# Kernel tuning notes

Hardware: AMD Instinct MI355X
Metric: run time of the kernel (lower is better)

## Reference

```python
import jax, jax.numpy as jnp
import numpy as np

B, IN_C, NHEAD, ATT_C, OUT_C, H, W = 512, 256, 8, 32, 32, 19, 19
EPS = 1e-5


def setup_inputs() -> dict:
    key = jax.random.key(0)
    ks = jax.random.split(key, 4)
    f32 = jnp.float32
    return {
        "x": jax.random.normal(ks[0], (B, IN_C, H, W), f32),
        "Wq": jax.random.normal(ks[1], (NHEAD * ATT_C, IN_C), f32) * 0.05,
        "bq": jnp.zeros((NHEAD * ATT_C,), f32),
        "Wk": jax.random.normal(ks[2], (NHEAD * ATT_C, IN_C), f32) * 0.05,
        "bk": jnp.zeros((NHEAD * ATT_C,), f32),
        "Wv": jax.random.normal(ks[3], (NHEAD * OUT_C, IN_C), f32) * 0.05,
        "bv": jnp.zeros((NHEAD * OUT_C,), f32),
        "gQ": jnp.ones((NHEAD * ATT_C,), f32),
        "betaQ": jnp.zeros((NHEAD * ATT_C,), f32),
        "gK": jnp.ones((NHEAD * ATT_C,), f32),
        "betaK": jnp.zeros((NHEAD * ATT_C,), f32),
        "gV": jnp.ones((NHEAD * OUT_C,), f32),
        "betaV": jnp.zeros((NHEAD * OUT_C,), f32),
    }


def _conv1x1(x, Wt, bt):
    # x: [B,Ci,H,W], Wt: [Co,Ci] -> [B,Co,H,W]
    return jnp.einsum("oi,bihw->bohw", Wt, x) + bt[None, :, None, None]


def _bn(x, g, b):
    # training-mode BatchNorm2d: batch stats over (N,H,W)
    mu = x.mean(axis=(0, 2, 3), keepdims=True)
    var = x.var(axis=(0, 2, 3), keepdims=True)
    return (x - mu) * jax.lax.rsqrt(var + EPS) * g[None, :, None, None] + b[None, :, None, None]


def _neighbors(t):
    # t: [B,C,H,W] -> [B,4,C,H,W] zero-padded 4-neighbor shifts (up,down,left,right)
    p = jnp.pad(t, ((0, 0), (0, 0), (1, 1), (1, 1)))
    return jnp.stack(
        (p[:, :, 0:-2, 1:-1], p[:, :, 2:, 1:-1], p[:, :, 1:-1, 0:-2], p[:, :, 1:-1, 2:]),
        axis=1,
    )


def reference(x, Wq, bq, Wk, bk, Wv, bv, gQ, betaQ, gK, betaK, gV, betaV):
    Q = _bn(_conv1x1(x, Wq, bq), gQ, betaQ)
    K = _bn(_conv1x1(x, Wk, bk), gK, betaK)
    V = _bn(_conv1x1(x, Wv, bv), gV, betaV)

    Kn = _neighbors(K).reshape(B, 4, NHEAD, ATT_C, H, W)
    Q4 = Q.reshape(B, 1, NHEAD, ATT_C, H, W)
    # attention logits: mean over att_c, then * sqrt(att_c)  (usenormmean == 0)
    a = (Q4 * Kn).mean(axis=3) * jnp.float32(ATT_C ** 0.5)  # [B,4,nhead,H,W]
    a = jax.nn.softmax(a, axis=1)[:, :, :, None]  # [B,4,nhead,1,H,W]

    Vn = _neighbors(V).reshape(B, 4, NHEAD, OUT_C, H, W)
    out = (a * Vn).sum(axis=1)  # [B,nhead,out_c,H,W]
    out = out.reshape(B, NHEAD * OUT_C, H, W)
    out = jax.nn.relu(out)  # useRelu == 1
    return out + x  # residual
```

## Files before the change

kernel.cpp:

```cpp
#include <hip/hip_runtime.h>

typedef unsigned short u16;
typedef unsigned int   u32;

#define NB     512
#define NHEADS 8
#define HW     361
#define NPIX   184832
#define NTOT   768
#define EPSBN  1e-5f
#define RS     0.17677669529663687f
#define PSTR   104

typedef __bf16 bf16x8 __attribute__((ext_vector_type(8)));
typedef float  f32x4  __attribute__((ext_vector_type(4)));

__device__ __forceinline__ u16 f2bf(float f) {
  u32 u = __float_as_uint(f);
  u += 0x7fffu + ((u >> 16) & 1u);
  return (u16)(u >> 16);
}
__device__ __forceinline__ float bf2f(u16 v) {
  return __uint_as_float(((u32)v) << 16);
}
__device__ __forceinline__ bf16x8 ldb8(const void* p) {
  return __builtin_bit_cast(bf16x8, *(const uint4*)p);
}
__device__ __forceinline__ float dot2(u32 a, u32 b) {
  return bf2f((u16)a) * bf2f((u16)b) + bf2f((u16)(a >> 16)) * bf2f((u16)(b >> 16));
}
__device__ __forceinline__ float dot8(uint4 a, uint4 b) {
  return dot2(a.x, b.x) + dot2(a.y, b.y) + dot2(a.z, b.z) + dot2(a.w, b.w);
}

__global__ __launch_bounds__(256) void k_prep(
    const float* __restrict__ Wq, const float* __restrict__ bq,
    const float* __restrict__ Wk, const float* __restrict__ bk,
    const float* __restrict__ Wv, const float* __restrict__ bv,
    u16* __restrict__ Wall, float* __restrict__ ball,
    float* __restrict__ sx) {
  const int n = blockIdx.x, t = threadIdx.x;
  const float* src; const float* bs; int r;
  if (n < 256)      { src = Wq; bs = bq; r = n; }
  else if (n < 512) { src = Wk; bs = bk; r = n - 256; }
  else              { src = Wv; bs = bv; r = n - 512; }
  Wall[n * 256 + t] = f2bf(src[r * 256 + t]);
  if (t == 0) ball[n] = bs[r];
  if (n == 0) sx[t] = 0.f;
}

__global__ __launch_bounds__(512) void k_M(
    const float* __restrict__ x, u16* __restrict__ xT,
    float* __restrict__ Mpart, float* __restrict__ sx) {
  __shared__ u16 Als[256 * 64];
  const int tid = threadIdx.x, g = blockIdx.x;
  const int lane = tid & 63, w = tid >> 6;
  const int l15 = lane & 15, kq = lane >> 4;
  const int sc  = tid >> 4;
  const int sq  = tid & 15;
  const int wpx = tid & 63;
  const int wcs = tid >> 6;
  char* Ab = (char*)Als;

  float sxp[8];
  f32x4 acc[2][16];
  #pragma unroll
  for (int i = 0; i < 8; ++i) sxp[i] = 0.f;
  #pragma unroll
  for (int f2 = 0; f2 < 16; ++f2) {
    acc[0][f2] = (f32x4){0.f, 0.f, 0.f, 0.f};
    acc[1][f2] = (f32x4){0.f, 0.f, 0.f, 0.f};
  }

  #pragma unroll 1
  for (int ch = 0; ch < 12; ++ch) {
    const int img = (ch >= 6) ? 1 : 0;
    const int px0 = (ch - img * 6) * 64;
    const int bb  = g * 2 + img;
    const int pb  = px0 + sq * 4;
    #pragma unroll
    for (int i = 0; i < 8; ++i) {
      const int c = sc + 32 * i;
      const float* xp = x + ((size_t)bb * 256 + c) * HW + pb;
      float v0, v1, v2, v3;
      if (pb + 3 < HW) {
        const float4 f4 = *(const float4*)xp;
        v0 = f4.x; v1 = f4.y; v2 = f4.z; v3 = f4.w;
      } else {
        v0 = (pb + 0 < HW) ? xp[0] : 0.f;
        v1 = (pb + 1 < HW) ? xp[1] : 0.f;
        v2 = (pb + 2 < HW) ? xp[2] : 0.f;
        v3 = (pb + 3 < HW) ? xp[3] : 0.f;
      }
      sxp[i] += v0 + v1 + v2 + v3;
      const u32 lo = (u32)f2bf(v0) | ((u32)f2bf(v1) << 16);
      const u32 hi = (u32)f2bf(v2) | ((u32)f2bf(v3) << 16);
      const int slot = (sq >> 1) ^ (c & 7);
      *(uint2*)(Ab + c * 128 + slot * 16 + (sq & 1) * 8) = make_uint2(lo, hi);
    }
    __syncthreads();
    #pragma unroll
    for (int kk = 0; kk < 2; ++kk) {
      const int gl = kk * 4 + kq;
      const int so = ((gl ^ (l15 & 7)) << 4);
      const int r0 = w * 32 + l15;
      const bf16x8 a0 = ldb8(Ab + r0 * 128 + so);
      const bf16x8 a1 = ldb8(Ab + (r0 + 16) * 128 + so);
      #pragma unroll
      for (int f2 = 0; f2 < 16; ++f2) {
        const bf16x8 b = ldb8(Ab + (f2 * 16 + l15) * 128 + so);
        acc[0][f2] = __builtin_amdgcn_mfma_f32_16x16x32_bf16(a0, b, acc[0][f2], 0, 0, 0);
        acc[1][f2] = __builtin_amdgcn_mfma_f32_16x16x32_bf16(a1, b, acc[1][f2], 0, 0, 0);
      }
    }
    const int pxg = px0 + wpx;
    if (pxg < HW) {
      __align__(16) u16 tmp[32];
      #pragma unroll
      for (int j = 0; j < 32; ++j) {
        const int c = wcs * 32 + j;
        tmp[j] = Als[c * 64 + (((wpx >> 3) ^ (c & 7)) << 3) + (wpx & 7)];
      }
      uint4* dst = (uint4*)(xT + ((size_t)bb * HW + pxg) * 256 + wcs * 32);
      dst[0] = ((const uint4*)tmp)[0];
      dst[1] = ((const uint4*)tmp)[1];
      dst[2] = ((const uint4*)tmp)[2];
      dst[3] = ((const uint4*)tmp)[3];
    }
    __syncthreads();
  }
  float* mp = Mpart + (size_t)g * 65536;
  #pragma unroll
  for (int f1 = 0; f1 < 2; ++f1)
    #pragma unroll
    for (int f2 = 0; f2 < 16; ++f2)
      #pragma unroll
      for (int j = 0; j < 4; ++j) {
        const int c1 = w * 32 + f1 * 16 + kq * 4 + j;
        const int c2 = f2 * 16 + l15;
        mp[c1 * 256 + c2] = acc[f1][f2][j];
      }
  #pragma unroll
  for (int i = 0; i < 8; ++i) {
    float v = sxp[i];
    v += __shfl_down(v, 8); v += __shfl_down(v, 4);
    v += __shfl_down(v, 2); v += __shfl_down(v, 1);
    if (sq == 0) atomicAdd(&sx[sc + 32 * i], v);
  }
}

__global__ __launch_bounds__(256) void k_red(const float* __restrict__ Mpart,
                                             float* __restrict__ Mg) {
  const int i = blockIdx.x * 256 + threadIdx.x;
  float s = 0.f;
  #pragma unroll 8
  for (int sl = 0; sl < 256; ++sl) s += Mpart[(size_t)sl * 65536 + i];
  Mg[i] = s;
}

__global__ __launch_bounds__(256) void k_stats2(
    const float* __restrict__ Mg, const float* __restrict__ sx,
    const float* __restrict__ Wq, const float* __restrict__ bq,
    const float* __restrict__ Wk, const float* __restrict__ bk,
    const float* __restrict__ Wv, const float* __restrict__ bv,
    const float* __restrict__ gQ, const float* __restrict__ betaQ,
    const float* __restrict__ gK, const float* __restrict__ betaK,
    const float* __restrict__ gV, const float* __restrict__ betaV,
    float* __restrict__ s_all, float* __restrict__ t_all) {
  __shared__ float ws[256];
  __shared__ float r1[4], r2[4];
  const int n = blockIdx.x, i = threadIdx.x;
  const int which = n >> 8, r = n & 255;
  const float* src = (which == 0) ? Wq : (which == 1) ? Wk : Wv;
  const float wi = src[r * 256 + i];
  ws[i] = wi;
  __syncthreads();
  float colsum = 0.f;
  #pragma unroll 4
  for (int j = 0; j < 256; ++j) colsum += Mg[j * 256 + i] * ws[j];
  float p1 = wi * sx[i];
  float p2 = wi * colsum;
  p1 += __shfl_down(p1, 32); p2 += __shfl_down(p2, 32);
  p1 += __shfl_down(p1, 16); p2 += __shfl_down(p2, 16);
  p1 += __shfl_down(p1, 8);  p2 += __shfl_down(p2, 8);
  p1 += __shfl_down(p1, 4);  p2 += __shfl_down(p2, 4);
  p1 += __shfl_down(p1, 2);  p2 += __shfl_down(p2, 2);
  p1 += __shfl_down(p1, 1);  p2 += __shfl_down(p2, 1);
  const int wv = i >> 6;
  if ((i & 63) == 0) { r1[wv] = p1; r2[wv] = p2; }
  __syncthreads();
  if (i == 0) {
    const float S1 = r1[0] + r1[1] + r1[2] + r1[3];
    const float S2 = r2[0] + r2[1] + r2[2] + r2[3];
    const float* bs = (which == 0) ? bq : (which == 1) ? bk : bv;
    const float* gs = (which == 0) ? gQ : (which == 1) ? gK : gV;
    const float* be = (which == 0) ? betaQ : (which == 1) ? betaK : betaV;
    const float b = bs[r];
    const float P = (float)NPIX;
    const float mean = (S1 + P * b) / P;
    const float Ey2  = (S2 + 2.f * b * S1 + P * b * b) / P;
    const float var  = Ey2 - mean * mean;
    const float s    = gs[r] * rsqrtf(var + EPSBN);
    s_all[n] = s;
    t_all[n] = be[r] - s * mean;
  }
}

__global__ __launch_bounds__(768) void k_fused(
    const u16* __restrict__ xT, const u16* __restrict__ Wall,
    const float* __restrict__ ball,
    const float* __restrict__ s_all, const float* __restrict__ t_all,
    const float* __restrict__ x, float* __restrict__ out) {
  __shared__ u16   Wl[96 * 256];
  __shared__ __align__(16) u16 P[HW * PSTR];
  __shared__ float aL[4 * HW];
  __shared__ float stl[2 * 96];
  const int tid = threadIdx.x;
  const int wg  = blockIdx.x;
  const int xcd = wg & 7, ii = wg >> 3;
  const int h   = ii & 7;
  const int pr  = xcd * 32 + (ii >> 3);
  const int bb0 = pr * 2;
  const char* Pb = (const char*)P;

  const int lane = tid & 63, wv = tid >> 6;
  const int l15 = lane & 15, kq = lane >> 4;

  const bool pact = tid < 2 * HW;
  const int  ppx  = pact ? ((tid < HW) ? tid : tid - HW) : 0;
  const int  poc0 = (tid < HW) ? 0 : 16;

  uint4 bfr[16];
  {
    const u16* xTb = xT + (size_t)bb0 * HW * 256;
    #pragma unroll
    for (int ks = 0; ks < 8; ++ks) {
      bfr[2 * ks]     = *(const uint4*)(xTb + (size_t)(wv * 32      + l15) * 256 + ks * 32 + kq * 8);
      bfr[2 * ks + 1] = *(const uint4*)(xTb + (size_t)(wv * 32 + 16 + l15) * 256 + ks * 32 + kq * 8);
    }
  }
  float xres[16];
  if (pact) {
    const size_t pg = ((size_t)bb0 * 256 + h * 32 + poc0) * HW + ppx;
    #pragma unroll
    for (int o = 0; o < 16; ++o) xres[o] = x[pg + (size_t)o * HW];
  }
  if (tid < 96) {
    const int which = tid >> 5, c32 = tid & 31;
    const int n = which * 256 + h * 32 + c32;
    float s = s_all[n];
    float t = s * ball[n] + t_all[n];
    if (tid < 32) { s *= RS; t *= RS; }
    stl[tid] = s; stl[96 + tid] = t;
  }
  #pragma unroll
  for (int i = 0; i < 4; ++i) {
    const int gi = tid + i * 768;
    const int lr = gi >> 5, gg = gi & 31;
    const int which = lr >> 5, c32 = lr & 31;
    uint4 v = *(const uint4*)(Wall + (size_t)(which * 256 + h * 32 + c32) * 256 + gg * 8);
    const int slot = gg ^ (lr & 7);
    *(uint4*)((char*)Wl + lr * 512 + slot * 16) = v;
  }
  __syncthreads();

  #pragma unroll
  for (int im = 0; im < 2; ++im) {
    const int bb = bb0 + im;
    f32x4 acc[6][2];
    #pragma unroll
    for (int f = 0; f < 6; ++f) {
      acc[f][0] = (f32x4){0.f, 0.f, 0.f, 0.f};
      acc[f][1] = (f32x4){0.f, 0.f, 0.f, 0.f};
    }
    #pragma unroll
    for (int ks = 0; ks < 8; ++ks) {
      bf16x8 b0 = __builtin_bit_cast(bf16x8, bfr[2 * ks]);
      bf16x8 b1 = __builtin_bit_cast(bf16x8, bfr[2 * ks + 1]);
      const int slot = ((ks * 4 + kq) ^ (l15 & 7)) * 16;
      #pragma unroll
      for (int f = 0; f < 6; ++f) {
        const int lr = (f >> 1) * 32 + (f & 1) * 16 + l15;
        bf16x8 a = ldb8((const char*)Wl + lr * 512 + slot);
        acc[f][0] = __builtin_amdgcn_mfma_f32_16x16x32_bf16(a, b0, acc[f][0], 0, 0, 0);
        acc[f][1] = __builtin_amdgcn_mfma_f32_16x16x32_bf16(a, b1, acc[f][1], 0, 0, 0);
      }
    }
    if (im == 0) {
      const u16* xTb2 = xT + (size_t)(bb0 + 1) * HW * 256;
      #pragma unroll
      for (int ks = 0; ks < 8; ++ks) {
        bfr[2 * ks]     = *(const uint4*)(xTb2 + (size_t)(wv * 32      + l15) * 256 + ks * 32 + kq * 8);
        bfr[2 * ks + 1] = *(const uint4*)(xTb2 + (size_t)(wv * 32 + 16 + l15) * 256 + ks * 32 + kq * 8);
      }
    }
    #pragma unroll
    for (int f = 0; f < 6; ++f) {
      const int ch0 = f * 16 + kq * 4;
      const float s0 = stl[ch0], t0 = stl[96 + ch0];
      const float s1 = stl[ch0 + 1], t1 = stl[96 + ch0 + 1];
      const float s2 = stl[ch0 + 2], t2 = stl[96 + ch0 + 2];
      const float s3 = stl[ch0 + 3], t3 = stl[96 + ch0 + 3];
      #pragma unroll
      for (int p2 = 0; p2 < 2; ++p2) {
        const int px = wv * 32 + p2 * 16 + l15;
        if (px < HW) {
          const u32 lo = (u32)f2bf(s0 * acc[f][p2][0] + t0)
                       | ((u32)f2bf(s1 * acc[f][p2][1] + t1) << 16);
          const u32 hi = (u32)f2bf(s2 * acc[f][p2][2] + t2)
                       | ((u32)f2bf(s3 * acc[f][p2][3] + t3) << 16);
          *(uint2*)((char*)P + px * 208 + f * 32 + kq * 8) = make_uint2(lo, hi);
        }
      }
    }
    __syncthreads();

    if (tid < HW) {
      const int px = tid;
      const int yy = px / 19, xx = px - yy * 19;
      const bool i0 = yy > 0, i1 = yy < 18, i2 = xx > 0, i3 = xx < 18;
      const int pn0 = i0 ? px - 19 : px, pn1 = i1 ? px + 19 : px;
      const int pn2 = i2 ? px - 1  : px, pn3 = i3 ? px + 1  : px;
      const uint4* Qp = (const uint4*)(Pb + px * 208);
      const uint4 q0 = Qp[0], q1 = Qp[1], q2 = Qp[2], q3 = Qp[3];
      const uint4* K0 = (const uint4*)(Pb + pn0 * 208 + 64);
      const uint4* K1 = (const uint4*)(Pb + pn1 * 208 + 64);
      const uint4* K2 = (const uint4*)(Pb + pn2 * 208 + 64);
      const uint4* K3 = (const uint4*)(Pb + pn3 * 208 + 64);
      float l0 = dot8(q0, K0[0]) + dot8(q1, K0[1]) + dot8(q2, K0[2]) + dot8(q3, K0[3]);
      float l1 = dot8(q0, K1[0]) + dot8(q1, K1[1]) + dot8(q2, K1[2]) + dot8(q3, K1[3]);
      float l2 = dot8(q0, K2[0]) + dot8(q1, K2[1]) + dot8(q2, K2[2]) + dot8(q3, K2[3]);
      float l3 = dot8(q0, K3[0]) + dot8(q1, K3[1]) + dot8(q2, K3[2]) + dot8(q3, K3[3]);
      l0 = i0 ? l0 : 0.f; l1 = i1 ? l1 : 0.f;
      l2 = i2 ? l2 : 0.f; l3 = i3 ? l3 : 0.f;
      const float mx = fmaxf(fmaxf(l0, l1), fmaxf(l2, l3));
      const float e0 = __expf(l0 - mx), e1 = __expf(l1 - mx);
      const float e2 = __expf(l2 - mx), e3 = __expf(l3 - mx);
      const float inv = 1.f / (e0 + e1 + e2 + e3);
      aL[0 * HW + px] = i0 ? e0 * inv : 0.f;
      aL[1 * HW + px] = i1 ? e1 * inv : 0.f;
      aL[2 * HW + px] = i2 ? e2 * inv : 0.f;
      aL[3 * HW + px] = i3 ? e3 * inv : 0.f;
    }
    __syncthreads();

    if (pact) {
      const int px = ppx;
      const size_t pgb = ((size_t)bb * 256 + h * 32 + poc0) * HW + px;
      const int yy = px / 19, xx = px - yy * 19;
      const int pn0 = (yy > 0)  ? px - 19 : px, pn1 = (yy < 18) ? px + 19 : px;
      const int pn2 = (xx > 0)  ? px - 1  : px, pn3 = (xx < 18) ? px + 1  : px;
      const float a0 = aL[0 * HW + px], a1 = aL[1 * HW + px];
      const float a2 = aL[2 * HW + px], a3 = aL[3 * HW + px];
      const int vb = 128 + poc0 * 2;
      const uint4* V0 = (const uint4*)(Pb + pn0 * 208 + vb);
      const uint4* V1 = (const uint4*)(Pb + pn1 * 208 + vb);
      const uint4* V2 = (const uint4*)(Pb + pn2 * 208 + vb);
      const uint4* V3 = (const uint4*)(Pb + pn3 * 208 + vb);
      #pragma unroll
      for (int half = 0; half < 2; ++half) {
        const uint4 w0 = V0[half], w1 = V1[half], w2 = V2[half], w3 = V3[half];
        const u32 u0[4] = {w0.x, w0.y, w0.z, w0.w};
        const u32 u1[4] = {w1.x, w1.y, w1.z, w1.w};
        const u32 u2[4] = {w2.x, w2.y, w2.z, w2.w};
        const u32 u3[4] = {w3.x, w3.y, w3.z, w3.w};
        #pragma unroll
        for (int p = 0; p < 4; ++p) {
          const int o = half * 8 + p * 2;
          float vlo = a0 * bf2f((u16)u0[p]) + a1 * bf2f((u16)u1[p])
                    + a2 * bf2f((u16)u2[p]) + a3 * bf2f((u16)u3[p]);
          float vhi = a0 * bf2f((u16)(u0[p] >> 16)) + a1 * bf2f((u16)(u1[p] >> 16))
                    + a2 * bf2f((u16)(u2[p] >> 16)) + a3 * bf2f((u16)(u3[p] >> 16));
          vlo = fmaxf(vlo, 0.f);
          vhi = fmaxf(vhi, 0.f);
          out[pgb + (size_t)o * HW]       = vlo + xres[o];
          out[pgb + (size_t)(o + 1) * HW] = vhi + xres[o + 1];
        }
      }
    }
    if (im == 0 && pact) {
      const size_t pg2 = ((size_t)(bb0 + 1) * 256 + h * 32 + poc0) * HW + ppx;
      #pragma unroll
      for (int o = 0; o < 16; ++o) xres[o] = x[pg2 + (size_t)o * HW];
    }
    __syncthreads();
  }
}

constexpr size_t OFF_XT    = 0;
constexpr size_t SZ_XT     = (size_t)NPIX * 512 + 16384;
constexpr size_t OFF_WALL  = OFF_XT + SZ_XT;
constexpr size_t SZ_WALL   = (size_t)NTOT * 512;
constexpr size_t OFF_BALL  = OFF_WALL + SZ_WALL;
constexpr size_t OFF_M     = OFF_BALL + NTOT * 4;
constexpr size_t SZ_M      = 256 * 256 * 4;
constexpr size_t OFF_SX    = OFF_M + SZ_M;
constexpr size_t OFF_SALL  = OFF_SX + 256 * 4;
constexpr size_t OFF_TALL  = OFF_SALL + NTOT * 4;
constexpr size_t OFF_MPART = OFF_TALL + NTOT * 4;
constexpr size_t SZ_MPART  = (size_t)256 * 65536 * 4;
constexpr size_t WS_NEEDED = OFF_MPART + SZ_MPART;

extern "C" void kernel_launch(void* const* d_in, const int* in_sizes, int n_in,
                              void* d_out, int out_size, void* d_ws, size_t ws_size,
                              hipStream_t stream) {
  (void)in_sizes; (void)n_in; (void)out_size;
  if (ws_size < WS_NEEDED) return;

  const float* x     = (const float*)d_in[0];
  const float* Wq    = (const float*)d_in[1];
  const float* bq    = (const float*)d_in[2];
  const float* Wk    = (const float*)d_in[3];
  const float* bk    = (const float*)d_in[4];
  const float* Wv    = (const float*)d_in[5];
  const float* bv    = (const float*)d_in[6];
  const float* gQ    = (const float*)d_in[7];
  const float* betaQ = (const float*)d_in[8];
  const float* gK    = (const float*)d_in[9];
  const float* betaK = (const float*)d_in[10];
  const float* gV    = (const float*)d_in[11];
  const float* betaV = (const float*)d_in[12];
  float* out = (float*)d_out;

  char* wsp = (char*)d_ws;
  u16*   xT    = (u16*)(wsp + OFF_XT);
  u16*   Wall  = (u16*)(wsp + OFF_WALL);
  float* ball  = (float*)(wsp + OFF_BALL);
  float* Mg    = (float*)(wsp + OFF_M);
  float* sx    = (float*)(wsp + OFF_SX);
  float* s_all = (float*)(wsp + OFF_SALL);
  float* t_all = (float*)(wsp + OFF_TALL);
  float* Mpart = (float*)(wsp + OFF_MPART);

  k_prep<<<NTOT, 256, 0, stream>>>(Wq, bq, Wk, bk, Wv, bv, Wall, ball, sx);
  k_M<<<256, 512, 0, stream>>>(x, xT, Mpart, sx);
  k_red<<<256, 256, 0, stream>>>(Mpart, Mg);
  k_stats2<<<NTOT, 256, 0, stream>>>(Mg, sx, Wq, bq, Wk, bk, Wv, bv,
                                     gQ, betaQ, gK, betaK, gV, betaV, s_all, t_all);
  k_fused<<<2048, 768, 0, stream>>>(xT, Wall, ball, s_all, t_all, x, out);
}
```

Baseline: 375.9 us.

## Split Gram-matrix kernel across two blocks per image pair with XCD-aware mapping

```diff
diff --git a/kernel.cpp b/kernel.cpp
--- a/kernel.cpp
+++ b/kernel.cpp
@@ -10,7 +10,6 @@
 #define NTOT   768
 #define EPSBN  1e-5f
 #define RS     0.17677669529663687f
-#define PSTR   104
 
 typedef __bf16 bf16x8 __attribute__((ext_vector_type(8)));
 typedef float  f32x4  __attribute__((ext_vector_type(4)));
@@ -53,7 +52,11 @@
     const float* __restrict__ x, u16* __restrict__ xT,
     float* __restrict__ Mpart, float* __restrict__ sx) {
   __shared__ u16 Als[256 * 64];
-  const int tid = threadIdx.x, g = blockIdx.x;
+  const int tid  = threadIdx.x;
+  const int orig = blockIdx.x;
+  const int xcd  = orig & 7, kk8 = orig >> 3;
+  const int g    = xcd * 32 + (kk8 >> 1);
+  const int half = kk8 & 1;
   const int lane = tid & 63, w = tid >> 6;
   const int l15 = lane & 15, kq = lane >> 4;
   const int sc  = tid >> 4;
@@ -61,16 +64,14 @@
   const int wpx = tid & 63;
   const int wcs = tid >> 6;
   char* Ab = (char*)Als;
+  const int c1base = half * 128 + w * 16;
 
   float sxp[8];
-  f32x4 acc[2][16];
+  f32x4 acc[16];
   #pragma unroll
   for (int i = 0; i < 8; ++i) sxp[i] = 0.f;
   #pragma unroll
-  for (int f2 = 0; f2 < 16; ++f2) {
-    acc[0][f2] = (f32x4){0.f, 0.f, 0.f, 0.f};
-    acc[1][f2] = (f32x4){0.f, 0.f, 0.f, 0.f};
-  }
+  for (int f2 = 0; f2 < 16; ++f2) acc[f2] = (f32x4){0.f, 0.f, 0.f, 0.f};
 
   #pragma unroll 1
   for (int ch = 0; ch < 12; ++ch) {
@@ -79,73 +80,78 @@
     const int bb  = g * 2 + img;
     const int pb  = px0 + sq * 4;
     #pragma unroll
-    for (int i = 0; i < 8; ++i) {
-      const int c = sc + 32 * i;
-      const float* xp = x + ((size_t)bb * 256 + c) * HW + pb;
-      float v0, v1, v2, v3;
-      if (pb + 3 < HW) {
-        const float4 f4 = *(const float4*)xp;
-        v0 = f4.x; v1 = f4.y; v2 = f4.z; v3 = f4.w;
-      } else {
-        v0 = (pb + 0 < HW) ? xp[0] : 0.f;
-        v1 = (pb + 1 < HW) ? xp[1] : 0.f;
-        v2 = (pb + 2 < HW) ? xp[2] : 0.f;
-        v3 = (pb + 3 < HW) ? xp[3] : 0.f;
-      }
-      sxp[i] += v0 + v1 + v2 + v3;
-      const u32 lo = (u32)f2bf(v0) | ((u32)f2bf(v1) << 16);
-      const u32 hi = (u32)f2bf(v2) | ((u32)f2bf(v3) << 16);
-      const int slot = (sq >> 1) ^ (c & 7);
-      *(uint2*)(Ab + c * 128 + slot * 16 + (sq & 1) * 8) = make_uint2(lo, hi);
+    for (int b4 = 0; b4 < 2; ++b4) {
+      float4 fv[4];
+      #pragma unroll
+      for (int i2 = 0; i2 < 4; ++i2) {
+        const int c = sc + 32 * (b4 * 4 + i2);
+        const float* xp = x + ((size_t)bb * 256 + c) * HW + pb;
+        if (pb + 3 < HW) {
+          fv[i2] = *(const float4*)xp;
+        } else {
+          fv[i2].x = (pb + 0 < HW) ? xp[0] : 0.f;
+          fv[i2].y = (pb + 1 < HW) ? xp[1] : 0.f;
+          fv[i2].z = (pb + 2 < HW) ? xp[2] : 0.f;
+          fv[i2].w = (pb + 3 < HW) ? xp[3] : 0.f;
+        }
+      }
+      #pragma unroll
+      for (int i2 = 0; i2 < 4; ++i2) {
+        const int i = b4 * 4 + i2;
+        const int c = sc + 32 * i;
+        sxp[i] += fv[i2].x + fv[i2].y + fv[i2].z + fv[i2].w;
+        const u32 lo = (u32)f2bf(fv[i2].x) | ((u32)f2bf(fv[i2].y) << 16);
+        const u32 hi = (u32)f2bf(fv[i2].z) | ((u32)f2bf(fv[i2].w) << 16);
+        const int slot = (sq >> 1) ^ (c & 7);
+        *(uint2*)(Ab + c * 128 + slot * 16 + (sq & 1) * 8) = make_uint2(lo, hi);
+      }
     }
     __syncthreads();
     #pragma unroll
     for (int kk = 0; kk < 2; ++kk) {
       const int gl = kk * 4 + kq;
       const int so = ((gl ^ (l15 & 7)) << 4);
-      const int r0 = w * 32 + l15;
-      const bf16x8 a0 = ldb8(Ab + r0 * 128 + so);
-      const bf16x8 a1 = ldb8(Ab + (r0 + 16) * 128 + so);
+      const bf16x8 a = ldb8(Ab + (c1base + l15) * 128 + so);
       #pragma unroll
       for (int f2 = 0; f2 < 16; ++f2) {
         const bf16x8 b = ldb8(Ab + (f2 * 16 + l15) * 128 + so);
-        acc[0][f2] = __builtin_amdgcn_mfma_f32_16x16x32_bf16(a0, b, acc[0][f2], 0, 0, 0);
-        acc[1][f2] = __builtin_amdgcn_mfma_f32_16x16x32_bf16(a1, b, acc[1][f2], 0, 0, 0);
-      }
-    }
-    const int pxg = px0 + wpx;
-    if (pxg < HW) {
-      __align__(16) u16 tmp[32];
-      #pragma unroll
-      for (int j = 0; j < 32; ++j) {
-        const int c = wcs * 32 + j;
-        tmp[j] = Als[c * 64 + (((wpx >> 3) ^ (c & 7)) << 3) + (wpx & 7)];
-      }
-      uint4* dst = (uint4*)(xT + ((size_t)bb * HW + pxg) * 256 + wcs * 32);
-      dst[0] = ((const uint4*)tmp)[0];
-      dst[1] = ((const uint4*)tmp)[1];
-      dst[2] = ((const uint4*)tmp)[2];
-      dst[3] = ((const uint4*)tmp)[3];
+        acc[f2] = __builtin_amdgcn_mfma_f32_16x16x32_bf16(a, b, acc[f2], 0, 0, 0);
+      }
+    }
+    if (half == 0) {
+      const int pxg = px0 + wpx;
+      if (pxg < HW) {
+        __align__(16) u16 tmp[32];
+        #pragma unroll
+        for (int j = 0; j < 32; ++j) {
+          const int c = wcs * 32 + j;
+          tmp[j] = Als[c * 64 + (((wpx >> 3) ^ (c & 7)) << 3) + (wpx & 7)];
+        }
+        uint4* dst = (uint4*)(xT + ((size_t)bb * HW + pxg) * 256 + wcs * 32);
+        dst[0] = ((const uint4*)tmp)[0];
+        dst[1] = ((const uint4*)tmp)[1];
+        dst[2] = ((const uint4*)tmp)[2];
+        dst[3] = ((const uint4*)tmp)[3];
+      }
     }
     __syncthreads();
   }
   float* mp = Mpart + (size_t)g * 65536;
   #pragma unroll
-  for (int f1 = 0; f1 < 2; ++f1)
-    #pragma unroll
-    for (int f2 = 0; f2 < 16; ++f2)
-      #pragma unroll
-      for (int j = 0; j < 4; ++j) {
-        const int c1 = w * 32 + f1 * 16 + kq * 4 + j;
-        const int c2 = f2 * 16 + l15;
-        mp[c1 * 256 + c2] = acc[f1][f2][j];
-      }
-  #pragma unroll
-  for (int i = 0; i < 8; ++i) {
-    float v = sxp[i];
-    v += __shfl_down(v, 8); v += __shfl_down(v, 4);
-    v += __shfl_down(v, 2); v += __shfl_down(v, 1);
-    if (sq == 0) atomicAdd(&sx[sc + 32 * i], v);
+  for (int f2 = 0; f2 < 16; ++f2)
+    #pragma unroll
+    for (int j = 0; j < 4; ++j) {
+      const int c1 = c1base + kq * 4 + j;
+      mp[c1 * 256 + f2 * 16 + l15] = acc[f2][j];
+    }
+  if (half == 0) {
+    #pragma unroll
+    for (int i = 0; i < 8; ++i) {
+      float v = sxp[i];
+      v += __shfl_down(v, 8); v += __shfl_down(v, 4);
+      v += __shfl_down(v, 2); v += __shfl_down(v, 1);
+      if (sq == 0) atomicAdd(&sx[sc + 32 * i], v);
+    }
   }
 }
 
@@ -212,7 +218,7 @@
     const float* __restrict__ s_all, const float* __restrict__ t_all,
     const float* __restrict__ x, float* __restrict__ out) {
   __shared__ u16   Wl[96 * 256];
-  __shared__ __align__(16) u16 P[HW * PSTR];
+  __shared__ __align__(16) u16 P[HW * 104];
   __shared__ float aL[4 * HW];
   __shared__ float stl[2 * 96];
   const int tid = threadIdx.x;
@@ -297,7 +303,7 @@
     #pragma unroll
     for (int f = 0; f < 6; ++f) {
       const int ch0 = f * 16 + kq * 4;
-      const float s0 = stl[ch0], t0 = stl[96 + ch0];
+      const float s0 = stl[ch0],     t0 = stl[96 + ch0];
       const float s1 = stl[ch0 + 1], t1 = stl[96 + ch0 + 1];
       const float s2 = stl[ch0 + 2], t2 = stl[96 + ch0 + 2];
       const float s3 = stl[ch0 + 3], t3 = stl[96 + ch0 + 3];
@@ -433,7 +439,7 @@
   float* Mpart = (float*)(wsp + OFF_MPART);
 
   k_prep<<<NTOT, 256, 0, stream>>>(Wq, bq, Wk, bk, Wv, bv, Wall, ball, sx);
-  k_M<<<256, 512, 0, stream>>>(x, xT, Mpart, sx);
+  k_M<<<512, 512, 0, stream>>>(x, xT, Mpart, sx);
   k_red<<<256, 256, 0, stream>>>(Mpart, Mg);
   k_stats2<<<NTOT, 256, 0, stream>>>(Mg, sx, Wq, bq, Wk, bk, Wv, bv,
                                      gQ, betaQ, gK, betaK, gV, betaV, s_all, t_all);
```

New measurement: 427.7 us. +13.8%, slower.
